# Optimization experiments

Measured on AMD Instinct MI355X. Metric: run time of the kernel, lower is better.

Reference implementation:

```python
import jax, jax.numpy as jnp
import numpy as np
import math

B, S, D = 16, 1024, 512
ALPHA = 1.0
DIRECTION = 'fw'


def masked_softmax(vec, mask):
    # faithful to the torch helper: multiply-by-mask, max-shift, exp, re-mask, normalize
    masked_vec = vec * mask
    max_vec = jnp.max(masked_vec, axis=2, keepdims=True)
    exps = jnp.exp(masked_vec - max_vec)
    masked_exps = exps * mask
    masked_sums = jnp.sum(masked_exps, axis=2, keepdims=True)
    masked_sums = masked_sums + (masked_sums == 0).astype(vec.dtype)
    return masked_exps / (masked_sums + 1e-20)


def setup_inputs() -> dict:
    key = jax.random.key(0)
    kq, kk, kv, km = jax.random.split(key, 4)
    q = jax.random.normal(kq, (B, S, D), dtype=jnp.float32)
    k = jax.random.normal(kk, (B, S, D), dtype=jnp.float32)
    v = jax.random.normal(kv, (B, S, D), dtype=jnp.float32)
    rep_mask = jax.random.randint(km, (B, S, 1), 0, 2, dtype=jnp.int32)
    return {"q": q, "k": k, "v": v, "rep_mask": rep_mask}


def reference(q, k, v, rep_mask):
    seq_len = q.shape[1]
    scale = jnp.asarray(math.sqrt(D), dtype=q.dtype)
    attention = jnp.einsum('bqd,bkd->bqk', q, k) / scale  # [B,S,S]

    ones = jnp.ones((seq_len, seq_len), dtype=q.dtype)
    if DIRECTION == 'fw':
        dir_mask = jnp.tril(ones, k=-1)
    else:
        dir_mask = jnp.triu(ones, k=1)

    rm = rep_mask.astype(q.dtype)                     # [B,S,1]
    rep = rm * jnp.swapaxes(rm, 1, 2)                 # [B,S,S]

    idx = jnp.arange(seq_len)
    dis_mask = -jnp.abs(idx[:, None] - idx[None, :]).astype(q.dtype)  # [S,S]

    mask = rep * dir_mask[None]                       # [B,S,S]
    attention = attention + ALPHA * dis_mask[None]
    attention = masked_softmax(attention, mask)
    out = jnp.einsum('bqk,bkd->bqd', attention, v)
    return (out, attention)
```

## Files before the change

### kernel.cpp

```cpp
#include <hip/hip_runtime.h>
#include <cstdint>

#define B_ 16
#define S_ 1024
#define D_ 512
#define TILE 128
#define BK 32
#define PITCH 36

typedef float f32x4 __attribute__((ext_vector_type(4)));
typedef short s16x8 __attribute__((ext_vector_type(8)));
typedef unsigned short u16;
typedef unsigned int u32;

__device__ __forceinline__ u16 f2bf(float f) {
    u32 u = __builtin_bit_cast(u32, f);
    u += 0x7FFFu + ((u >> 16) & 1u);
    return (u16)(u >> 16);
}


#define GLD16(g, l) __builtin_amdgcn_global_load_lds( \
    (const __attribute__((address_space(1))) u32*)(g), \
    (__attribute__((address_space(3))) u32*)(l), 16, 0, 0)

__global__ __launch_bounds__(256) void cvt2_kernel(const float* __restrict__ q,
                                                   const float* __restrict__ k,
                                                   u16* __restrict__ Qb,
                                                   u16* __restrict__ Kb) {
    const float* src = blockIdx.y ? k : q;
    u16* dst = blockIdx.y ? Kb : Qb;
    int i = (blockIdx.x * 256 + threadIdx.x) * 8;
    float4 a = *(const float4*)(src + i);
    float4 b = *(const float4*)(src + i + 4);
    union { ushort4 h[2]; s16x8 v; } r;
    r.h[0] = make_ushort4(f2bf(a.x), f2bf(a.y), f2bf(a.z), f2bf(a.w));
    r.h[1] = make_ushort4(f2bf(b.x), f2bf(b.y), f2bf(b.z), f2bf(b.w));
    *(s16x8*)(dst + i) = r.v;
}

#define TP 66
__global__ __launch_bounds__(256) void trv_kernel(const float* __restrict__ v,
                                                  u16* __restrict__ vt) {
    const int d0 = blockIdx.x * 64, j0 = blockIdx.y * 64, b = blockIdx.z;
    __shared__ u16 t[64 * TP];
    const int tid = threadIdx.x;
    const int tj = tid >> 2;
    const int td = (tid & 3) * 16;
    const float* src = v + ((size_t)b * S_ + j0 + tj) * D_ + d0 + td;
#pragma unroll
    for (int e = 0; e < 4; ++e) {
        float4 a = *(const float4*)(src + e * 4);
        *(ushort4*)(t + tj * TP + td + e * 4) =
            make_ushort4(f2bf(a.x), f2bf(a.y), f2bf(a.z), f2bf(a.w));
    }
    __syncthreads();
    const int dd = tid >> 2;
    const int jj = (tid & 3) * 16;
    u16* dstp = vt + ((size_t)b * D_ + d0 + dd) * S_ + j0 + jj;
    u16 tmp[16];
#pragma unroll
    for (int e = 0; e < 16; ++e) tmp[e] = t[(jj + e) * TP + dd];
    *(s16x8*)dstp = *(s16x8*)tmp;
    *(s16x8*)(dstp + 8) = *(s16x8*)(tmp + 8);
}

__device__ __forceinline__ s16x8 frag_swz(const u16* lds, int row, int colbyte) {
    int off = row * 128 + (colbyte ^ ((row & 7) << 4));
    return *(const s16x8*)((const char*)lds + off);
}

__device__ __forceinline__ void gemm_body(const u16* ag, const u16* bg, int lda, int ldb,
                                          int nk, u16* lA, u16* lB, f32x4 acc[4][4],
                                          int tid) {
    const int lane = tid & 63, wid = tid >> 6;
    const int l8 = lane >> 3, l7 = lane & 7;
    const int cswz = (l7 ^ l8) * 8;
    const u16* ga[4];
    const u16* gb[4];
#pragma unroll
    for (int q2 = 0; q2 < 4; ++q2) {
        int seg = wid * 4 + q2;
        int row = seg * 8 + l8;
        ga[q2] = ag + (size_t)row * lda + cswz;
        gb[q2] = bg + (size_t)row * ldb + cswz;
    }
    const int wr = (wid >> 1) * 64, wc = (wid & 1) * 64;
    const int r15 = lane & 15;
    const int cb = (lane >> 4) * 16;

    for (int kk = 0; kk < nk; kk += 64) {
#pragma unroll
        for (int q2 = 0; q2 < 4; ++q2) {
            int seg = wid * 4 + q2;
            GLD16(ga[q2] + kk, lA + seg * 512);
            GLD16(gb[q2] + kk, lB + seg * 512);
        }
        __syncthreads();
#pragma unroll
        for (int ks = 0; ks < 2; ++ks) {
            s16x8 af[4], bf4[4];
#pragma unroll
            for (int m = 0; m < 4; ++m) af[m] = frag_swz(lA, wr + m * 16 + r15, ks * 64 + cb);
#pragma unroll
            for (int n = 0; n < 4; ++n) bf4[n] = frag_swz(lB, wc + n * 16 + r15, ks * 64 + cb);
#pragma unroll
            for (int m = 0; m < 4; ++m)
#pragma unroll
                for (int n = 0; n < 4; ++n)
                    acc[m][n] = __builtin_amdgcn_mfma_f32_16x16x32_bf16(af[m], bf4[n], acc[m][n], 0, 0, 0);
        }
        __syncthreads();
    }
}

__global__ __launch_bounds__(256) void qk2_kernel(const u16* __restrict__ Qb,
                                                  const u16* __restrict__ Kb,
                                                  float* __restrict__ attn) {
    const int bid = blockIdx.x;
    const int xcd = bid & 7;
    const int w = bid >> 3;
    const int b = xcd * 2 + (w & 1);
    int p = w >> 1;
    int qt = 0, tri = 0;
    while (p >= tri + qt + 1) { tri += qt + 1; ++qt; }
    const int kt = p - tri;

    __shared__ u16 lA[128 * 64];
    __shared__ u16 lB[128 * 64];
    const int tid = threadIdx.x, lane = tid & 63, wid = tid >> 6;
    f32x4 acc[4][4] = {};
    gemm_body(Qb + ((size_t)b * S_ + (size_t)qt * 128) * D_,
              Kb + ((size_t)b * S_ + (size_t)kt * 128) * D_,
              D_, D_, D_, lA, lB, acc, tid);
    const float scale = 0.04419417382415922f;
    const int wr = (wid >> 1) * 64, wc = (wid & 1) * 64;
    const int r15 = lane & 15, rr = (lane >> 4) * 4;
    size_t base = ((size_t)b * S_ + (size_t)qt * 128) * S_ + (size_t)kt * 128;
#pragma unroll
    for (int m = 0; m < 4; ++m)
#pragma unroll
        for (int n = 0; n < 4; ++n)
#pragma unroll
            for (int r = 0; r < 4; ++r)
                attn[base + (size_t)(wr + m * 16 + rr + r) * S_ + wc + n * 16 + r15] =
                    acc[m][n][r] * scale;
}

__global__ __launch_bounds__(256) void pv2_kernel(const u16* __restrict__ Pb,
                                                  const u16* __restrict__ Vt,
                                                  float* __restrict__ out) {
    const int bid = blockIdx.x;
    const int xcd = bid & 7;
    const int w = bid >> 3;
    const int b = xcd * 2 + (w & 1);
    const int r = w >> 1;
    const int dt = r & 3, qt = r >> 2;

    __shared__ u16 lA[128 * 64];
    __shared__ u16 lB[128 * 64];
    const int tid = threadIdx.x, lane = tid & 63, wid = tid >> 6;
    f32x4 acc[4][4] = {};
    gemm_body(Pb + ((size_t)b * S_ + (size_t)qt * 128) * S_,
              Vt + ((size_t)b * D_ + (size_t)dt * 128) * S_,
              S_, S_, (qt + 1) * 128, lA, lB, acc, tid);
    const int wr = (wid >> 1) * 64, wc = (wid & 1) * 64;
    const int r15 = lane & 15, rr = (lane >> 4) * 4;
    size_t base = ((size_t)b * S_ + (size_t)qt * 128) * D_ + (size_t)dt * 128;
#pragma unroll
    for (int m = 0; m < 4; ++m)
#pragma unroll
        for (int n = 0; n < 4; ++n)
#pragma unroll
            for (int rg = 0; rg < 4; ++rg)
                out[base + (size_t)(wr + m * 16 + rr + rg) * D_ + wc + n * 16 + r15] =
                    acc[m][n][rg];
}

__global__ __launch_bounds__(256) void sm_kernel(const int* __restrict__ rep_mask,
                                                 float* __restrict__ attn,
                                                 u16* __restrict__ pb) {
    const int i = blockIdx.x, b = blockIdx.y;
    const int tid = threadIdx.x;
    const int lane = tid & 63, wid = tid >> 6;
    float* row = attn + ((size_t)b * S_ + i) * S_;
    const int* rm = rep_mask + (size_t)b * S_;
    __shared__ float red[8];

    const int mi = rm[i];
    const int j0 = tid * 4;
    int4 m4 = ((const int4*)rm)[tid];
    float4 lv = make_float4(0.f, 0.f, 0.f, 0.f);
    if (mi != 0 && j0 < i) lv = *(const float4*)(row + j0);

    const int mv[4] = {m4.x, m4.y, m4.z, m4.w};
    const float lf[4] = {lv.x, lv.y, lv.z, lv.w};
    float vec[4];
    bool val[4];
    float mymax = 0.0f;
#pragma unroll
    for (int e = 0; e < 4; ++e) {
        int j = j0 + e;
        val[e] = (mi != 0) && (j < i) && (mv[e] != 0);
        vec[e] = lf[e] - (float)(i - j);
        if (val[e]) mymax = fmaxf(mymax, vec[e]);
    }
#pragma unroll
    for (int off = 32; off > 0; off >>= 1) mymax = fmaxf(mymax, __shfl_down(mymax, off));
    if (lane == 0) red[wid] = mymax;
    __syncthreads();
    const float m = fmaxf(fmaxf(red[0], red[1]), fmaxf(red[2], red[3]));

    float ex[4];
    float mysum = 0.0f;
#pragma unroll
    for (int e = 0; e < 4; ++e) {
        ex[e] = val[e] ? expf(vec[e] - m) : 0.0f;
        mysum += ex[e];
    }
#pragma unroll
    for (int off = 32; off > 0; off >>= 1) mysum += __shfl_down(mysum, off);
    if (lane == 0) red[4 + wid] = mysum;
    __syncthreads();
    const float ssum = red[4] + red[5] + red[6] + red[7];
    const float denom = ssum + (ssum == 0.0f ? 1.0f : 0.0f) + 1e-20f;
    const float inv = 1.0f / denom;
    float4 o = make_float4(ex[0] * inv, ex[1] * inv, ex[2] * inv, ex[3] * inv);
    *(float4*)(row + j0) = o;
    if (pb != nullptr && j0 <= (i | 127)) {
        u16* pr = pb + ((size_t)b * S_ + i) * S_ + j0;
        *(ushort4*)pr = make_ushort4(f2bf(o.x), f2bf(o.y), f2bf(o.z), f2bf(o.w));
    }
}


union Frag { s16x8 v; uint2 u[2]; };

__device__ __forceinline__ s16x8 load_frag(const u16* lds, int row, int kq) {
    Frag f;
    const u16* p = lds + row * PITCH + kq;
    f.u[0] = *(const uint2*)p;
    f.u[1] = *(const uint2*)(p + 4);
    return f.v;
}

__device__ __forceinline__ void stage_granule(u16* lds, const float* src, int ldsrc, int g) {
    int row = g >> 2;
    int c8 = (g & 3) * 8;
    const float4* s = (const float4*)(src + (size_t)row * ldsrc + c8);
    float4 x0 = s[0], x1 = s[1];
    *(ushort4*)(lds + row * PITCH + c8) =
        make_ushort4(f2bf(x0.x), f2bf(x0.y), f2bf(x0.z), f2bf(x0.w));
    *(ushort4*)(lds + row * PITCH + c8 + 4) =
        make_ushort4(f2bf(x1.x), f2bf(x1.y), f2bf(x1.z), f2bf(x1.w));
}

__global__ __launch_bounds__(256) void qk_kernel(const float* __restrict__ q,
                                                 const float* __restrict__ k,
                                                 float* __restrict__ attn) {
    const int kt = blockIdx.x, qt = blockIdx.y, b = blockIdx.z;
    if (kt > qt) return;
    __shared__ u16 lA[TILE * PITCH];
    __shared__ u16 lB[TILE * PITCH];
    const int tid = threadIdx.x;
    const int lane = tid & 63;
    const int wid = tid >> 6;
    const int wr = (wid >> 1) * 64, wc = (wid & 1) * 64;
    const int r15 = lane & 15, kq = (lane >> 4) * 8;
    const float* qb = q + ((size_t)b * S_ + (size_t)qt * TILE) * D_;
    const float* kb = k + ((size_t)b * S_ + (size_t)kt * TILE) * D_;
    f32x4 acc[4][4] = {};
    for (int kk = 0; kk < D_; kk += BK) {
        __syncthreads();
        stage_granule(lA, qb + kk, D_, tid);
        stage_granule(lA, qb + kk, D_, tid + 256);
        stage_granule(lB, kb + kk, D_, tid);
        stage_granule(lB, kb + kk, D_, tid + 256);
        __syncthreads();
        s16x8 af[4], bf[4];
#pragma unroll
        for (int m = 0; m < 4; ++m) af[m] = load_frag(lA, wr + m * 16 + r15, kq);
#pragma unroll
        for (int n = 0; n < 4; ++n) bf[n] = load_frag(lB, wc + n * 16 + r15, kq);
#pragma unroll
        for (int m = 0; m < 4; ++m)
#pragma unroll
            for (int n = 0; n < 4; ++n)
                acc[m][n] = __builtin_amdgcn_mfma_f32_16x16x32_bf16(af[m], bf[n], acc[m][n], 0, 0, 0);
    }
    const float scale = 0.04419417382415922f;
    size_t base = ((size_t)b * S_ + (size_t)qt * TILE) * S_ + (size_t)kt * TILE;
    const int rr = (lane >> 4) * 4;
#pragma unroll
    for (int m = 0; m < 4; ++m)
#pragma unroll
        for (int n = 0; n < 4; ++n)
#pragma unroll
            for (int r = 0; r < 4; ++r)
                attn[base + (size_t)(wr + m * 16 + rr + r) * S_ + wc + n * 16 + r15] =
                    acc[m][n][r] * scale;
}

__global__ __launch_bounds__(256) void pv_kernel(const float* __restrict__ attn,
                                                 const float* __restrict__ v,
                                                 float* __restrict__ out) {
    const int dt = blockIdx.x, qt = blockIdx.y, b = blockIdx.z;
    __shared__ u16 lP[TILE * PITCH];
    __shared__ u16 lV[TILE * PITCH];
    const int tid = threadIdx.x;
    const int lane = tid & 63;
    const int wid = tid >> 6;
    const int wr = (wid >> 1) * 64, wc = (wid & 1) * 64;
    const int r15 = lane & 15, kq = (lane >> 4) * 8;
    const float* pb = attn + ((size_t)b * S_ + (size_t)qt * TILE) * S_;
    const float* vb = v + (size_t)b * S_ * D_ + (size_t)dt * TILE;
    const int vd0 = (tid & 31) * 4;
    const int vj0 = (tid >> 5) * 4;
    f32x4 acc[4][4] = {};
    const int nk = (qt + 1) * TILE;
    for (int kk = 0; kk < nk; kk += BK) {
        __syncthreads();
        stage_granule(lP, pb + kk, S_, tid);
        stage_granule(lP, pb + kk, S_, tid + 256);
        {
            const float* vs = vb + (size_t)(kk + vj0) * D_ + vd0;
            float4 r0 = *(const float4*)vs;
            float4 r1 = *(const float4*)(vs + D_);
            float4 r2 = *(const float4*)(vs + 2 * D_);
            float4 r3 = *(const float4*)(vs + 3 * D_);
            *(ushort4*)(lV + (vd0 + 0) * PITCH + vj0) = make_ushort4(f2bf(r0.x), f2bf(r1.x), f2bf(r2.x), f2bf(r3.x));
            *(ushort4*)(lV + (vd0 + 1) * PITCH + vj0) = make_ushort4(f2bf(r0.y), f2bf(r1.y), f2bf(r2.y), f2bf(r3.y));
            *(ushort4*)(lV + (vd0 + 2) * PITCH + vj0) = make_ushort4(f2bf(r0.z), f2bf(r1.z), f2bf(r2.z), f2bf(r3.z));
            *(ushort4*)(lV + (vd0 + 3) * PITCH + vj0) = make_ushort4(f2bf(r0.w), f2bf(r1.w), f2bf(r2.w), f2bf(r3.w));
        }
        __syncthreads();
        s16x8 af[4], bf[4];
#pragma unroll
        for (int m = 0; m < 4; ++m) af[m] = load_frag(lP, wr + m * 16 + r15, kq);
#pragma unroll
        for (int n = 0; n < 4; ++n) bf[n] = load_frag(lV, wc + n * 16 + r15, kq);
#pragma unroll
        for (int m = 0; m < 4; ++m)
#pragma unroll
            for (int n = 0; n < 4; ++n)
                acc[m][n] = __builtin_amdgcn_mfma_f32_16x16x32_bf16(af[m], bf[n], acc[m][n], 0, 0, 0);
    }
    size_t base = ((size_t)b * S_ + (size_t)qt * TILE) * D_ + (size_t)dt * TILE;
    const int rr = (lane >> 4) * 4;
#pragma unroll
    for (int m = 0; m < 4; ++m)
#pragma unroll
        for (int n = 0; n < 4; ++n)
#pragma unroll
            for (int r = 0; r < 4; ++r)
                out[base + (size_t)(wr + m * 16 + rr + r) * D_ + wc + n * 16 + r15] =
                    acc[m][n][r];
}

extern "C" void kernel_launch(void* const* d_in, const int* in_sizes, int n_in,
                              void* d_out, int out_size, void* d_ws, size_t ws_size,
                              hipStream_t stream) {
    const float* q = (const float*)d_in[0];
    const float* k = (const float*)d_in[1];
    const float* v = (const float*)d_in[2];
    const int* rep = (const int*)d_in[3];
    float* out = (float*)d_out;
    float* attn = out + (size_t)B_ * S_ * D_;

    const size_t nqk = (size_t)B_ * S_ * D_;
    const size_t need = 3 * nqk * sizeof(u16);
    if (ws_size >= need) {
        u16* Qb = (u16*)d_ws;
        u16* Kb = Qb + nqk;
        u16* Vt = Kb + nqk;
        u16* Pb = (u16*)d_ws;
        cvt2_kernel<<<dim3(nqk / (8 * 256), 2), 256, 0, stream>>>(q, k, Qb, Kb);
        trv_kernel<<<dim3(D_ / 64, S_ / 64, B_), 256, 0, stream>>>(v, Vt);
        qk2_kernel<<<8 * 72, 256, 0, stream>>>(Qb, Kb, attn);
        sm_kernel<<<dim3(S_, B_), 256, 0, stream>>>(rep, attn, Pb);
        pv2_kernel<<<8 * 64, 256, 0, stream>>>(Pb, Vt, out);
    } else {
        qk_kernel<<<dim3(S_ / TILE, S_ / TILE, B_), 256, 0, stream>>>(q, k, attn);
        sm_kernel<<<dim3(S_, B_), 256, 0, stream>>>(rep, attn, nullptr);
        pv_kernel<<<dim3(D_ / TILE, S_ / TILE, B_), 256, 0, stream>>>(attn, v, out);
    }
}
```

Before: 92.37 us.

## Fuse softmax stats into QK epilogue and normalization into PV kernel

The QK kernel now applies the direction, rep and distance masks in its epilogue. It computes per-tile row max and sum-of-exp partials into a small workspace buffer. A new fin kernel merges those partials per row, normalizes the attention row in place, and writes zeros for masked rows and upper tiles. It converts the probabilities to bf16 in LDS and runs the PV MFMA with V fragments read directly from global memory. The bf16 conversion of Q and K and the transpose of V are also merged into one launch. This removes the separate softmax pass and its extra read/write of the attention matrix and bf16 P buffer, at the cost of lower V reuse (16-row blocks) and more global traffic for the V fragments.

```diff
diff --git a/kernel.cpp b/kernel.cpp
--- a/kernel.cpp
+++ b/kernel.cpp
@@ -19,50 +19,52 @@
     return (u16)(u >> 16);
 }
 
-
 #define GLD16(g, l) __builtin_amdgcn_global_load_lds( \
     (const __attribute__((address_space(1))) u32*)(g), \
     (__attribute__((address_space(3))) u32*)(l), 16, 0, 0)
 
-__global__ __launch_bounds__(256) void cvt2_kernel(const float* __restrict__ q,
+#define TP 66
+__global__ __launch_bounds__(256) void prep_kernel(const float* __restrict__ q,
                                                    const float* __restrict__ k,
+                                                   const float* __restrict__ v,
                                                    u16* __restrict__ Qb,
-                                                   u16* __restrict__ Kb) {
-    const float* src = blockIdx.y ? k : q;
-    u16* dst = blockIdx.y ? Kb : Qb;
-    int i = (blockIdx.x * 256 + threadIdx.x) * 8;
-    float4 a = *(const float4*)(src + i);
-    float4 b = *(const float4*)(src + i + 4);
-    union { ushort4 h[2]; s16x8 v; } r;
-    r.h[0] = make_ushort4(f2bf(a.x), f2bf(a.y), f2bf(a.z), f2bf(a.w));
-    r.h[1] = make_ushort4(f2bf(b.x), f2bf(b.y), f2bf(b.z), f2bf(b.w));
-    *(s16x8*)(dst + i) = r.v;
-}
-
-#define TP 66
-__global__ __launch_bounds__(256) void trv_kernel(const float* __restrict__ v,
-                                                  u16* __restrict__ vt) {
-    const int d0 = blockIdx.x * 64, j0 = blockIdx.y * 64, b = blockIdx.z;
+                                                   u16* __restrict__ Kb,
+                                                   u16* __restrict__ Vt) {
     __shared__ u16 t[64 * TP];
+    const int bid = blockIdx.x;
     const int tid = threadIdx.x;
-    const int tj = tid >> 2;
-    const int td = (tid & 3) * 16;
-    const float* src = v + ((size_t)b * S_ + j0 + tj) * D_ + d0 + td;
-#pragma unroll
-    for (int e = 0; e < 4; ++e) {
-        float4 a = *(const float4*)(src + e * 4);
-        *(ushort4*)(t + tj * TP + td + e * 4) =
-            make_ushort4(f2bf(a.x), f2bf(a.y), f2bf(a.z), f2bf(a.w));
-    }
-    __syncthreads();
-    const int dd = tid >> 2;
-    const int jj = (tid & 3) * 16;
-    u16* dstp = vt + ((size_t)b * D_ + d0 + dd) * S_ + j0 + jj;
-    u16 tmp[16];
-#pragma unroll
-    for (int e = 0; e < 16; ++e) tmp[e] = t[(jj + e) * TP + dd];
-    *(s16x8*)dstp = *(s16x8*)tmp;
-    *(s16x8*)(dstp + 8) = *(s16x8*)(tmp + 8);
+    if (bid < 8192) {
+        const float* src = (bid < 4096) ? q : k;
+        u16* dst = (bid < 4096) ? Qb : Kb;
+        int i = (((bid & 4095) * 256) + tid) * 8;
+        float4 a = *(const float4*)(src + i);
+        float4 b2 = *(const float4*)(src + i + 4);
+        union { ushort4 h[2]; s16x8 v; } r;
+        r.h[0] = make_ushort4(f2bf(a.x), f2bf(a.y), f2bf(a.z), f2bf(a.w));
+        r.h[1] = make_ushort4(f2bf(b2.x), f2bf(b2.y), f2bf(b2.z), f2bf(b2.w));
+        *(s16x8*)(dst + i) = r.v;
+    } else {
+        int tt = bid - 8192;
+        const int d0 = (tt & 7) * 64, j0 = ((tt >> 3) & 15) * 64, b = tt >> 7;
+        const int tj = tid >> 2;
+        const int td = (tid & 3) * 16;
+        const float* src = v + ((size_t)b * S_ + j0 + tj) * D_ + d0 + td;
+#pragma unroll
+        for (int e = 0; e < 4; ++e) {
+            float4 a = *(const float4*)(src + e * 4);
+            *(ushort4*)(t + tj * TP + td + e * 4) =
+                make_ushort4(f2bf(a.x), f2bf(a.y), f2bf(a.z), f2bf(a.w));
+        }
+        __syncthreads();
+        const int dd = tid >> 2;
+        const int jj = (tid & 3) * 16;
+        u16* dstp = Vt + ((size_t)b * D_ + d0 + dd) * S_ + j0 + jj;
+        u16 tmp[16];
+#pragma unroll
+        for (int e = 0; e < 16; ++e) tmp[e] = t[(jj + e) * TP + dd];
+        *(s16x8*)dstp = *(s16x8*)tmp;
+        *(s16x8*)(dstp + 8) = *(s16x8*)(tmp + 8);
+    }
 }
 
 __device__ __forceinline__ s16x8 frag_swz(const u16* lds, int row, int colbyte) {
@@ -114,9 +116,11 @@
     }
 }
 
-__global__ __launch_bounds__(256) void qk2_kernel(const u16* __restrict__ Qb,
+__global__ __launch_bounds__(256) void qk3_kernel(const u16* __restrict__ Qb,
                                                   const u16* __restrict__ Kb,
-                                                  float* __restrict__ attn) {
+                                                  const int* __restrict__ rep,
+                                                  float* __restrict__ attn,
+                                                  float2* __restrict__ st) {
     const int bid = blockIdx.x;
     const int xcd = bid & 7;
     const int w = bid >> 3;
@@ -128,109 +132,168 @@
 
     __shared__ u16 lA[128 * 64];
     __shared__ u16 lB[128 * 64];
+    __shared__ int lrepr[128];
+    __shared__ int lrepc[128];
+    __shared__ float lst[2][64][2][2];
+
     const int tid = threadIdx.x, lane = tid & 63, wid = tid >> 6;
+    if (tid < 128) lrepr[tid] = rep[(size_t)b * S_ + qt * 128 + tid];
+    else lrepc[tid - 128] = rep[(size_t)b * S_ + kt * 128 + (tid - 128)];
+
     f32x4 acc[4][4] = {};
     gemm_body(Qb + ((size_t)b * S_ + (size_t)qt * 128) * D_,
               Kb + ((size_t)b * S_ + (size_t)kt * 128) * D_,
               D_, D_, D_, lA, lB, acc, tid);
+
     const float scale = 0.04419417382415922f;
     const int wr = (wid >> 1) * 64, wc = (wid & 1) * 64;
-    const int r15 = lane & 15, rr = (lane >> 4) * 4;
+    const int r15 = lane & 15, g4 = lane >> 4;
     size_t base = ((size_t)b * S_ + (size_t)qt * 128) * S_ + (size_t)kt * 128;
+
 #pragma unroll
     for (int m = 0; m < 4; ++m)
 #pragma unroll
-        for (int n = 0; n < 4; ++n)
-#pragma unroll
-            for (int r = 0; r < 4; ++r)
-                attn[base + (size_t)(wr + m * 16 + rr + r) * S_ + wc + n * 16 + r15] =
-                    acc[m][n][r] * scale;
-}
-
-__global__ __launch_bounds__(256) void pv2_kernel(const u16* __restrict__ Pb,
+        for (int r = 0; r < 4; ++r) {
+            const int row = wr + m * 16 + g4 * 4 + r;
+            const int gi = qt * 128 + row;
+            const int im = lrepr[row];
+            float vv[4];
+            float mx = 0.0f;
+#pragma unroll
+            for (int n = 0; n < 4; ++n) {
+                const int col = wc + n * 16 + r15;
+                const int gj = kt * 128 + col;
+                const bool val = im && (gj < gi) && (lrepc[col] != 0);
+                float v = acc[m][n][r] * scale - (float)(gi - gj);
+                vv[n] = val ? v : -1e30f;
+                if (val) mx = fmaxf(mx, v);
+            }
+            if (im) {
+#pragma unroll
+                for (int n = 0; n < 4; ++n)
+                    attn[base + (size_t)row * S_ + wc + n * 16 + r15] = vv[n];
+            }
+#pragma unroll
+            for (int off = 1; off < 16; off <<= 1)
+                mx = fmaxf(mx, __shfl_xor(mx, off));
+            float sm = 0.0f;
+#pragma unroll
+            for (int n = 0; n < 4; ++n)
+                if (vv[n] > -1e29f) sm += __expf(vv[n] - mx);
+#pragma unroll
+            for (int off = 1; off < 16; off <<= 1)
+                sm += __shfl_xor(sm, off);
+            if (r15 == 0) {
+                lst[wid >> 1][m * 16 + g4 * 4 + r][wid & 1][0] = mx;
+                lst[wid >> 1][m * 16 + g4 * 4 + r][wid & 1][1] = sm;
+            }
+        }
+    __syncthreads();
+    if (tid < 128) {
+        const int wr2 = tid >> 6, row = tid & 63;
+        float m0 = lst[wr2][row][0][0], s0 = lst[wr2][row][0][1];
+        float m1 = lst[wr2][row][1][0], s1 = lst[wr2][row][1][1];
+        float M = fmaxf(m0, m1);
+        float S = s0 * __expf(m0 - M) + s1 * __expf(m1 - M);
+        const int gi = qt * 128 + wr2 * 64 + row;
+        st[(((size_t)b * 8 + kt) << 10) + gi] = make_float2(M, S);
+    }
+}
+
+__global__ __launch_bounds__(256) void fin_kernel(const float2* __restrict__ st,
+                                                  const int* __restrict__ rep,
                                                   const u16* __restrict__ Vt,
+                                                  float* __restrict__ attn,
                                                   float* __restrict__ out) {
     const int bid = blockIdx.x;
-    const int xcd = bid & 7;
-    const int w = bid >> 3;
+    const int xcd = bid & 7, w = bid >> 3;
     const int b = xcd * 2 + (w & 1);
-    const int r = w >> 1;
-    const int dt = r & 3, qt = r >> 2;
-
-    __shared__ u16 lA[128 * 64];
-    __shared__ u16 lB[128 * 64];
+    const int t = w >> 1;
+    const int qc = ((t & 7) << 3) | (t >> 3);
+    const int i0 = qc * 16;
+    const int nct = (qc >> 3) + 1;
+
+    __shared__ u16 lP[16 * 128];
+    __shared__ float lM[16], lI[16];
+    __shared__ int lmi[16];
+
     const int tid = threadIdx.x, lane = tid & 63, wid = tid >> 6;
-    f32x4 acc[4][4] = {};
-    gemm_body(Pb + ((size_t)b * S_ + (size_t)qt * 128) * S_,
-              Vt + ((size_t)b * D_ + (size_t)dt * 128) * S_,
-              S_, S_, (qt + 1) * 128, lA, lB, acc, tid);
-    const int wr = (wid >> 1) * 64, wc = (wid & 1) * 64;
-    const int r15 = lane & 15, rr = (lane >> 4) * 4;
-    size_t base = ((size_t)b * S_ + (size_t)qt * 128) * D_ + (size_t)dt * 128;
-#pragma unroll
-    for (int m = 0; m < 4; ++m)
-#pragma unroll
-        for (int n = 0; n < 4; ++n)
-#pragma unroll
-            for (int rg = 0; rg < 4; ++rg)
-                out[base + (size_t)(wr + m * 16 + rr + rg) * D_ + wc + n * 16 + r15] =
-                    acc[m][n][rg];
-}
-
-__global__ __launch_bounds__(256) void sm_kernel(const int* __restrict__ rep_mask,
-                                                 float* __restrict__ attn,
-                                                 u16* __restrict__ pb) {
-    const int i = blockIdx.x, b = blockIdx.y;
-    const int tid = threadIdx.x;
-    const int lane = tid & 63, wid = tid >> 6;
-    float* row = attn + ((size_t)b * S_ + i) * S_;
-    const int* rm = rep_mask + (size_t)b * S_;
-    __shared__ float red[8];
-
-    const int mi = rm[i];
-    const int j0 = tid * 4;
-    int4 m4 = ((const int4*)rm)[tid];
-    float4 lv = make_float4(0.f, 0.f, 0.f, 0.f);
-    if (mi != 0 && j0 < i) lv = *(const float4*)(row + j0);
-
-    const int mv[4] = {m4.x, m4.y, m4.z, m4.w};
-    const float lf[4] = {lv.x, lv.y, lv.z, lv.w};
-    float vec[4];
-    bool val[4];
-    float mymax = 0.0f;
-#pragma unroll
-    for (int e = 0; e < 4; ++e) {
-        int j = j0 + e;
-        val[e] = (mi != 0) && (j < i) && (mv[e] != 0);
-        vec[e] = lf[e] - (float)(i - j);
-        if (val[e]) mymax = fmaxf(mymax, vec[e]);
-    }
-#pragma unroll
-    for (int off = 32; off > 0; off >>= 1) mymax = fmaxf(mymax, __shfl_down(mymax, off));
-    if (lane == 0) red[wid] = mymax;
+    const int r15 = lane & 15, g4 = lane >> 4;
+
+    if (tid < 16) {
+        const int gi = i0 + tid;
+        float M = 0.0f, S = 0.0f;
+        for (int kt = 0; kt < nct; ++kt) {
+            float2 ms = st[(((size_t)b * 8 + kt) << 10) + gi];
+            float Mn = fmaxf(M, ms.x);
+            S = S * __expf(M - Mn) + ms.y * __expf(ms.x - Mn);
+            M = Mn;
+        }
+        float denom = (S == 0.0f ? 1.0f : S) + 1e-20f;
+        lM[tid] = M;
+        lI[tid] = 1.0f / denom;
+        lmi[tid] = rep[(size_t)b * S_ + gi];
+    }
     __syncthreads();
-    const float m = fmaxf(fmaxf(red[0], red[1]), fmaxf(red[2], red[3]));
-
-    float ex[4];
-    float mysum = 0.0f;
-#pragma unroll
-    for (int e = 0; e < 4; ++e) {
-        ex[e] = val[e] ? expf(vec[e] - m) : 0.0f;
-        mysum += ex[e];
-    }
-#pragma unroll
-    for (int off = 32; off > 0; off >>= 1) mysum += __shfl_down(mysum, off);
-    if (lane == 0) red[4 + wid] = mysum;
-    __syncthreads();
-    const float ssum = red[4] + red[5] + red[6] + red[7];
-    const float denom = ssum + (ssum == 0.0f ? 1.0f : 0.0f) + 1e-20f;
-    const float inv = 1.0f / denom;
-    float4 o = make_float4(ex[0] * inv, ex[1] * inv, ex[2] * inv, ex[3] * inv);
-    *(float4*)(row + j0) = o;
-    if (pb != nullptr && j0 <= (i | 127)) {
-        u16* pr = pb + ((size_t)b * S_ + i) * S_ + j0;
-        *(ushort4*)pr = make_ushort4(f2bf(o.x), f2bf(o.y), f2bf(o.z), f2bf(o.w));
-    }
+
+    float* aw = attn + ((size_t)b * S_ + i0) * S_;
+    const u16* vtb = Vt + (size_t)b * D_ * S_;
+    const int row16 = tid >> 4, u = tid & 15;
+
+    f32x4 acc[8] = {};
+    for (int c = 0; c < 8; ++c) {
+        if (c < nct) {
+            __syncthreads();
+            float pvv[8];
+            if (lmi[row16]) {
+                const float* src = aw + (size_t)row16 * S_ + c * 128 + u * 8;
+                float4 x0 = *(const float4*)src;
+                float4 x1 = *(const float4*)(src + 4);
+                const float M = lM[row16], I = lI[row16];
+                pvv[0] = __expf(x0.x - M) * I; pvv[1] = __expf(x0.y - M) * I;
+                pvv[2] = __expf(x0.z - M) * I; pvv[3] = __expf(x0.w - M) * I;
+                pvv[4] = __expf(x1.x - M) * I; pvv[5] = __expf(x1.y - M) * I;
+                pvv[6] = __expf(x1.z - M) * I; pvv[7] = __expf(x1.w - M) * I;
+            } else {
+#pragma unroll
+                for (int e = 0; e < 8; ++e) pvv[e] = 0.0f;
+            }
+            float* dst = aw + (size_t)row16 * S_ + c * 128 + u * 8;
+            *(float4*)dst = make_float4(pvv[0], pvv[1], pvv[2], pvv[3]);
+            *(float4*)(dst + 4) = make_float4(pvv[4], pvv[5], pvv[6], pvv[7]);
+            {
+                union { ushort4 h[2]; s16x8 v; } r;
+                r.h[0] = make_ushort4(f2bf(pvv[0]), f2bf(pvv[1]), f2bf(pvv[2]), f2bf(pvv[3]));
+                r.h[1] = make_ushort4(f2bf(pvv[4]), f2bf(pvv[5]), f2bf(pvv[6]), f2bf(pvv[7]));
+                const int half = u >> 3, colb = (u & 7) * 16;
+                *(s16x8*)((char*)lP + (row16 * 2 + half) * 128 + (colb ^ ((row16 & 7) << 4))) = r.v;
+            }
+            __syncthreads();
+#pragma unroll
+            for (int ks = 0; ks < 4; ++ks) {
+                const int half = ks >> 1, colb = (ks & 1) * 64 + g4 * 16;
+                s16x8 pa = *(const s16x8*)((const char*)lP +
+                             (r15 * 2 + half) * 128 + (colb ^ ((r15 & 7) << 4)));
+#pragma unroll
+                for (int nf = 0; nf < 8; ++nf) {
+                    s16x8 vb = *(const s16x8*)(vtb +
+                        (size_t)(wid * 128 + nf * 16 + r15) * S_ + c * 128 + ks * 32 + g4 * 8);
+                    acc[nf] = __builtin_amdgcn_mfma_f32_16x16x32_bf16(pa, vb, acc[nf], 0, 0, 0);
+                }
+            }
+        } else {
+            float* dst = aw + (size_t)row16 * S_ + c * 128 + u * 8;
+            *(float4*)dst = make_float4(0.f, 0.f, 0.f, 0.f);
+            *(float4*)(dst + 4) = make_float4(0.f, 0.f, 0.f, 0.f);
+        }
+    }
+
+    float* ob = out + ((size_t)b * S_ + i0) * D_;
+#pragma unroll
+    for (int nf = 0; nf < 8; ++nf)
+#pragma unroll
+        for (int rg = 0; rg < 4; ++rg)
+            ob[(size_t)(g4 * 4 + rg) * D_ + wid * 128 + nf * 16 + r15] = acc[nf][rg];
 }
 
 
@@ -299,6 +362,53 @@
             for (int r = 0; r < 4; ++r)
                 attn[base + (size_t)(wr + m * 16 + rr + r) * S_ + wc + n * 16 + r15] =
                     acc[m][n][r] * scale;
+}
+
+__global__ __launch_bounds__(256) void sm_kernel(const int* __restrict__ rep_mask,
+                                                 float* __restrict__ attn) {
+    const int i = blockIdx.x, b = blockIdx.y;
+    const int tid = threadIdx.x;
+    const int lane = tid & 63, wid = tid >> 6;
+    float* row = attn + ((size_t)b * S_ + i) * S_;
+    const int* rm = rep_mask + (size_t)b * S_;
+    __shared__ float red[8];
+    const int mi = rm[i];
+    const int j0 = tid * 4;
+    int4 m4 = ((const int4*)rm)[tid];
+    float4 lv = make_float4(0.f, 0.f, 0.f, 0.f);
+    if (mi != 0 && j0 < i) lv = *(const float4*)(row + j0);
+    const int mv[4] = {m4.x, m4.y, m4.z, m4.w};
+    const float lf[4] = {lv.x, lv.y, lv.z, lv.w};
+    float vec[4];
+    bool val[4];
+    float mymax = 0.0f;
+#pragma unroll
+    for (int e = 0; e < 4; ++e) {
+        int j = j0 + e;
+        val[e] = (mi != 0) && (j < i) && (mv[e] != 0);
+        vec[e] = lf[e] - (float)(i - j);
+        if (val[e]) mymax = fmaxf(mymax, vec[e]);
+    }
+#pragma unroll
+    for (int off = 32; off > 0; off >>= 1) mymax = fmaxf(mymax, __shfl_down(mymax, off));
+    if (lane == 0) red[wid] = mymax;
+    __syncthreads();
+    const float m = fmaxf(fmaxf(red[0], red[1]), fmaxf(red[2], red[3]));
+    float ex[4];
+    float mysum = 0.0f;
+#pragma unroll
+    for (int e = 0; e < 4; ++e) {
+        ex[e] = val[e] ? expf(vec[e] - m) : 0.0f;
+        mysum += ex[e];
+    }
+#pragma unroll
+    for (int off = 32; off > 0; off >>= 1) mysum += __shfl_down(mysum, off);
+    if (lane == 0) red[4 + wid] = mysum;
+    __syncthreads();
+    const float ssum = red[4] + red[5] + red[6] + red[7];
+    const float denom = ssum + (ssum == 0.0f ? 1.0f : 0.0f) + 1e-20f;
+    const float inv = 1.0f / denom;
+    *(float4*)(row + j0) = make_float4(ex[0] * inv, ex[1] * inv, ex[2] * inv, ex[3] * inv);
 }
 
 __global__ __launch_bounds__(256) void pv_kernel(const float* __restrict__ attn,
@@ -368,20 +478,19 @@
     float* attn = out + (size_t)B_ * S_ * D_;
 
     const size_t nqk = (size_t)B_ * S_ * D_;
-    const size_t need = 3 * nqk * sizeof(u16);
+    const size_t nst = (size_t)B_ * 8 * S_;
+    const size_t need = 3 * nqk * sizeof(u16) + nst * sizeof(float2);
     if (ws_size >= need) {
         u16* Qb = (u16*)d_ws;
         u16* Kb = Qb + nqk;
         u16* Vt = Kb + nqk;
-        u16* Pb = (u16*)d_ws;
-        cvt2_kernel<<<dim3(nqk / (8 * 256), 2), 256, 0, stream>>>(q, k, Qb, Kb);
-        trv_kernel<<<dim3(D_ / 64, S_ / 64, B_), 256, 0, stream>>>(v, Vt);
-        qk2_kernel<<<8 * 72, 256, 0, stream>>>(Qb, Kb, attn);
-        sm_kernel<<<dim3(S_, B_), 256, 0, stream>>>(rep, attn, Pb);
-        pv2_kernel<<<8 * 64, 256, 0, stream>>>(Pb, Vt, out);
+        float2* st = (float2*)(Vt + nqk);
+        prep_kernel<<<10240, 256, 0, stream>>>(q, k, v, Qb, Kb, Vt);
+        qk3_kernel<<<8 * 72, 256, 0, stream>>>(Qb, Kb, rep, attn, st);
+        fin_kernel<<<1024, 256, 0, stream>>>(st, rep, Vt, attn, out);
     } else {
         qk_kernel<<<dim3(S_ / TILE, S_ / TILE, B_), 256, 0, stream>>>(q, k, attn);
-        sm_kernel<<<dim3(S_, B_), 256, 0, stream>>>(rep, attn, nullptr);
+        sm_kernel<<<dim3(S_, B_), 256, 0, stream>>>(rep, attn);
         pv_kernel<<<dim3(D_ / TILE, S_ / TILE, B_), 256, 0, stream>>>(attn, v, out);
     }
 }
```

After: 164.5 us. 78.1% more time.

## Fuse prep kernels, skip masked-row stores in QK, schedule heavy tiles first

Applied to the files above, without the earlier changes.

Merges the Q/K bf16 conversion and the V transpose into one launch, removing one kernel launch. The QK kernel now loads the row mask and writes score rows only where rep_mask is nonzero, which cuts global store traffic because the softmax kernel presumably rewrites masked rows anyway. The QK and PV tile orders are reversed so the largest causal tiles are scheduled first, for better load balance. The store skip depends on sm_kernel not reading unwritten rows.

```diff
diff --git a/kernel.cpp b/kernel.cpp
--- a/kernel.cpp
+++ b/kernel.cpp
@@ -19,50 +19,52 @@
     return (u16)(u >> 16);
 }
 
-
 #define GLD16(g, l) __builtin_amdgcn_global_load_lds( \
     (const __attribute__((address_space(1))) u32*)(g), \
     (__attribute__((address_space(3))) u32*)(l), 16, 0, 0)
 
-__global__ __launch_bounds__(256) void cvt2_kernel(const float* __restrict__ q,
+#define TP 66
+__global__ __launch_bounds__(256) void prep_kernel(const float* __restrict__ q,
                                                    const float* __restrict__ k,
+                                                   const float* __restrict__ v,
                                                    u16* __restrict__ Qb,
-                                                   u16* __restrict__ Kb) {
-    const float* src = blockIdx.y ? k : q;
-    u16* dst = blockIdx.y ? Kb : Qb;
-    int i = (blockIdx.x * 256 + threadIdx.x) * 8;
-    float4 a = *(const float4*)(src + i);
-    float4 b = *(const float4*)(src + i + 4);
-    union { ushort4 h[2]; s16x8 v; } r;
-    r.h[0] = make_ushort4(f2bf(a.x), f2bf(a.y), f2bf(a.z), f2bf(a.w));
-    r.h[1] = make_ushort4(f2bf(b.x), f2bf(b.y), f2bf(b.z), f2bf(b.w));
-    *(s16x8*)(dst + i) = r.v;
-}
-
-#define TP 66
-__global__ __launch_bounds__(256) void trv_kernel(const float* __restrict__ v,
-                                                  u16* __restrict__ vt) {
-    const int d0 = blockIdx.x * 64, j0 = blockIdx.y * 64, b = blockIdx.z;
+                                                   u16* __restrict__ Kb,
+                                                   u16* __restrict__ Vt) {
     __shared__ u16 t[64 * TP];
+    const int bid = blockIdx.x;
     const int tid = threadIdx.x;
-    const int tj = tid >> 2;
-    const int td = (tid & 3) * 16;
-    const float* src = v + ((size_t)b * S_ + j0 + tj) * D_ + d0 + td;
-#pragma unroll
-    for (int e = 0; e < 4; ++e) {
-        float4 a = *(const float4*)(src + e * 4);
-        *(ushort4*)(t + tj * TP + td + e * 4) =
-            make_ushort4(f2bf(a.x), f2bf(a.y), f2bf(a.z), f2bf(a.w));
-    }
-    __syncthreads();
-    const int dd = tid >> 2;
-    const int jj = (tid & 3) * 16;
-    u16* dstp = vt + ((size_t)b * D_ + d0 + dd) * S_ + j0 + jj;
-    u16 tmp[16];
-#pragma unroll
-    for (int e = 0; e < 16; ++e) tmp[e] = t[(jj + e) * TP + dd];
-    *(s16x8*)dstp = *(s16x8*)tmp;
-    *(s16x8*)(dstp + 8) = *(s16x8*)(tmp + 8);
+    if (bid < 8192) {
+        const float* src = (bid < 4096) ? q : k;
+        u16* dst = (bid < 4096) ? Qb : Kb;
+        int i = (((bid & 4095) * 256) + tid) * 8;
+        float4 a = *(const float4*)(src + i);
+        float4 b2 = *(const float4*)(src + i + 4);
+        union { ushort4 h[2]; s16x8 v; } r;
+        r.h[0] = make_ushort4(f2bf(a.x), f2bf(a.y), f2bf(a.z), f2bf(a.w));
+        r.h[1] = make_ushort4(f2bf(b2.x), f2bf(b2.y), f2bf(b2.z), f2bf(b2.w));
+        *(s16x8*)(dst + i) = r.v;
+    } else {
+        int tt = bid - 8192;
+        const int d0 = (tt & 7) * 64, j0 = ((tt >> 3) & 15) * 64, b = tt >> 7;
+        const int tj = tid >> 2;
+        const int td = (tid & 3) * 16;
+        const float* src = v + ((size_t)b * S_ + j0 + tj) * D_ + d0 + td;
+#pragma unroll
+        for (int e = 0; e < 4; ++e) {
+            float4 a = *(const float4*)(src + e * 4);
+            *(ushort4*)(t + tj * TP + td + e * 4) =
+                make_ushort4(f2bf(a.x), f2bf(a.y), f2bf(a.z), f2bf(a.w));
+        }
+        __syncthreads();
+        const int dd = tid >> 2;
+        const int jj = (tid & 3) * 16;
+        u16* dstp = Vt + ((size_t)b * D_ + d0 + dd) * S_ + j0 + jj;
+        u16 tmp[16];
+#pragma unroll
+        for (int e = 0; e < 16; ++e) tmp[e] = t[(jj + e) * TP + dd];
+        *(s16x8*)dstp = *(s16x8*)tmp;
+        *(s16x8*)(dstp + 8) = *(s16x8*)(tmp + 8);
+    }
 }
 
 __device__ __forceinline__ s16x8 frag_swz(const u16* lds, int row, int colbyte) {
@@ -116,19 +118,23 @@
 
 __global__ __launch_bounds__(256) void qk2_kernel(const u16* __restrict__ Qb,
                                                   const u16* __restrict__ Kb,
+                                                  const int* __restrict__ rep,
                                                   float* __restrict__ attn) {
     const int bid = blockIdx.x;
     const int xcd = bid & 7;
     const int w = bid >> 3;
     const int b = xcd * 2 + (w & 1);
-    int p = w >> 1;
+    int p = 35 - (w >> 1);
     int qt = 0, tri = 0;
     while (p >= tri + qt + 1) { tri += qt + 1; ++qt; }
     const int kt = p - tri;
 
     __shared__ u16 lA[128 * 64];
     __shared__ u16 lB[128 * 64];
+    __shared__ int lrepr[128];
     const int tid = threadIdx.x, lane = tid & 63, wid = tid >> 6;
+    if (tid < 128) lrepr[tid] = rep[(size_t)b * S_ + qt * 128 + tid];
+
     f32x4 acc[4][4] = {};
     gemm_body(Qb + ((size_t)b * S_ + (size_t)qt * 128) * D_,
               Kb + ((size_t)b * S_ + (size_t)kt * 128) * D_,
@@ -140,11 +146,15 @@
 #pragma unroll
     for (int m = 0; m < 4; ++m)
 #pragma unroll
-        for (int n = 0; n < 4; ++n)
-#pragma unroll
-            for (int r = 0; r < 4; ++r)
-                attn[base + (size_t)(wr + m * 16 + rr + r) * S_ + wc + n * 16 + r15] =
-                    acc[m][n][r] * scale;
+        for (int r = 0; r < 4; ++r) {
+            const int row = wr + m * 16 + rr + r;
+            if (lrepr[row]) {
+#pragma unroll
+                for (int n = 0; n < 4; ++n)
+                    attn[base + (size_t)row * S_ + wc + n * 16 + r15] =
+                        acc[m][n][r] * scale;
+            }
+        }
 }
 
 __global__ __launch_bounds__(256) void pv2_kernel(const u16* __restrict__ Pb,
@@ -155,7 +165,7 @@
     const int w = bid >> 3;
     const int b = xcd * 2 + (w & 1);
     const int r = w >> 1;
-    const int dt = r & 3, qt = r >> 2;
+    const int dt = r & 3, qt = 7 - (r >> 2);
 
     __shared__ u16 lA[128 * 64];
     __shared__ u16 lB[128 * 64];
@@ -374,9 +384,8 @@
         u16* Kb = Qb + nqk;
         u16* Vt = Kb + nqk;
         u16* Pb = (u16*)d_ws;
-        cvt2_kernel<<<dim3(nqk / (8 * 256), 2), 256, 0, stream>>>(q, k, Qb, Kb);
-        trv_kernel<<<dim3(D_ / 64, S_ / 64, B_), 256, 0, stream>>>(v, Vt);
-        qk2_kernel<<<8 * 72, 256, 0, stream>>>(Qb, Kb, attn);
+        prep_kernel<<<10240, 256, 0, stream>>>(q, k, v, Qb, Kb, Vt);
+        qk2_kernel<<<8 * 72, 256, 0, stream>>>(Qb, Kb, rep, attn);
         sm_kernel<<<dim3(S_, B_), 256, 0, stream>>>(rep, attn, Pb);
         pv2_kernel<<<8 * 64, 256, 0, stream>>>(Pb, Vt, out);
     } else {
```

Result: faster. 90.05 us (median of 2 runs) (-2.5%).
